# Kernel optimization log

Hardware: AMD Instinct MI355X
Metric: run time of the kernel (lower is better)

The kernel has to match this reference:

```python
import jax, jax.numpy as jnp
import numpy as np

B, N, C, H = 8, 512, 64, 128
T, K = 10, 2                       # dilation threshold and skip divisor
TAUS = (0.25, 0.5, 0.75)
WTS = (0.25, 0.5, 0.25)
EPS_GIN = 0.0                      # (1 + eps) * x, eps buffer
AVG_DEG = 32.0


def setup_inputs() -> dict:
    key = jax.random.key(0)
    ks = jax.random.split(key, 6)
    x = jax.random.normal(ks[0], (B, N, C), jnp.float32)
    u = jax.random.uniform(ks[1], (B, N, N))
    a = u < (AVG_DEG / N)
    adj = jnp.maximum(a, jnp.swapaxes(a, 1, 2)).astype(jnp.float32)  # symmetric binary adjacency
    mask = jax.random.bernoulli(ks[2], 0.9, (B, N))
    W1 = jax.random.normal(ks[3], (C, H), jnp.float32) / np.float32(np.sqrt(C))
    b1 = jnp.zeros((H,), jnp.float32)
    W2 = jax.random.normal(ks[4], (H, C), jnp.float32) / np.float32(np.sqrt(H))
    b2 = jnp.zeros((C,), jnp.float32)
    return {"x": x, "adj": adj, "mask": mask, "W1": W1, "b1": b1, "W2": W2, "b2": b2}


def reference(x, adj, mask, W1, b1, W2, b2):
    Bc, Nc, Cc = x.shape
    eye = jnp.eye(Nc, dtype=bool)
    adj_ = jnp.where(eye, 1.0, adj)                 # add_loop=True: force self loops
    # ---- vectorized dilation (replaces the per-(b,n) python loop) ----
    neigh = (adj_ > 0) & (~eye)                     # neighbors excluding self [B,N,N]
    ni = neigh.astype(jnp.int32)
    rank = jnp.cumsum(ni, axis=-1) - ni             # exclusive rank of m among n's sorted neighbors
    nb = ni.sum(-1)                                 # [B,N] neighbor count (w/o self)
    skip = jnp.where(nb > T, (nb + K - 1) // K, 1)  # ceil(nb/k) if nb > T else 1 (linear mode, layer 1)
    skip = jnp.maximum(skip, 1)
    sk = skip[:, :, None]
    # remove relative indices skip-1, 2*skip-1, ... when skip > 1, only for masked-in nodes
    rem = neigh & (sk > 1) & ((rank % sk) == (sk - 1)) & mask[:, :, None]
    rem = rem | jnp.swapaxes(rem, 1, 2)             # symmetric removal
    adj_d = jnp.where(rem, 0.0, adj_)
    # ---- masked quantile aggregation over neighbors (== nanquantile) ----
    nd = adj_d > 0                                  # includes self loop -> at least 1 valid
    vals = jnp.where(nd[..., None], x[:, None, :, :], jnp.inf)  # [B,N,M,C]; invalid -> +inf
    s = jnp.sort(vals, axis=2)                      # valid values first, ascending
    nv = nd.sum(2)                                  # [B,N] valid count per node
    agg = jnp.zeros_like(x)
    for tau, w in zip(TAUS, WTS):                   # small fixed loop over quantiles
        pos = jnp.asarray(tau, x.dtype) * jnp.maximum(nv - 1, 0).astype(x.dtype)
        lo = jnp.floor(pos).astype(jnp.int32)
        hi = jnp.ceil(pos).astype(jnp.int32)
        frac = (pos - lo.astype(x.dtype))[..., None]
        idx_lo = jnp.broadcast_to(lo[:, :, None, None], (Bc, Nc, 1, Cc))
        idx_hi = jnp.broadcast_to(hi[:, :, None, None], (Bc, Nc, 1, Cc))
        v_lo = jnp.take_along_axis(s, idx_lo, axis=2)[:, :, 0, :]
        v_hi = jnp.take_along_axis(s, idx_hi, axis=2)[:, :, 0, :]
        agg = agg + jnp.asarray(w, x.dtype) * (v_lo + frac * (v_hi - v_lo))
    agg = jnp.where(nv[..., None] > 0, agg, 0.0)    # nan_to_num for empty rows
    out = (1.0 + EPS_GIN) * x + agg
    h = jax.nn.relu(out @ W1 + b1)                  # GIN MLP: Linear-ReLU-Linear
    y = h @ W2 + b2
    return y * mask[..., None].astype(y.dtype)
```

## Files before the change

### kernel.cpp

```cpp
#include <hip/hip_runtime.h>
#include <cstdint>

#define B_ 8
#define N_ 512
#define C_ 64
#define H_ 128
#define T_ 10
#define K_ 2
#define WPR 16
#define NVMAX 96
#define TT 8

__device__ inline uint32_t fkey(float v) {
    uint32_t bits = __float_as_uint(v);
    return (bits & 0x80000000u) ? ~bits : (bits | 0x80000000u);
}
__device__ inline float fdec(uint32_t key) {
    uint32_t ok = (key & 0xFFFFFF00u) | 0x80u;
    uint32_t bits = (ok & 0x80000000u) ? (ok ^ 0x80000000u) : ~ok;
    return __uint_as_float(bits);
}

__global__ __launch_bounds__(256) void pass1_rem(const float* __restrict__ adj,
                                                 const int* __restrict__ mask,
                                                 uint32_t* __restrict__ rembits) {
    int wid = threadIdx.x >> 6, lane = threadIdx.x & 63;
    int row = blockIdx.x * 4 + wid;
    int i = row & (N_ - 1);
    const float4* arow4 = (const float4*)(adj + (size_t)row * N_);
    float4 a0 = arow4[lane * 2];
    float4 a1 = arow4[lane * 2 + 1];
    float av[8] = {a0.x, a0.y, a0.z, a0.w, a1.x, a1.y, a1.z, a1.w};

    int flags = 0, cnt = 0;
    int jbase = lane * 8;
#pragma unroll
    for (int k = 0; k < 8; ++k) {
        int j = jbase + k;
        bool ng = (j != i) && (av[k] > 0.0f);
        flags |= ((int)ng) << k;
        cnt += (int)ng;
    }
    int inc = cnt;
#pragma unroll
    for (int d = 1; d < 64; d <<= 1) {
        int o = __shfl_up(inc, d, 64);
        if (lane >= d) inc += o;
    }
    int excl = inc - cnt;
    int nb = __shfl(inc, 63, 64);
    int skip = (nb > T_) ? ((nb + K_ - 1) / K_) : 1;
    if (skip < 1) skip = 1;
    int maski = mask[row];

    unsigned byteval = 0;
    if (skip > 1 && maski != 0) {
        int r = excl;
#pragma unroll
        for (int k = 0; k < 8; ++k) {
            if ((flags >> k) & 1) {
                if (r % skip == skip - 1) byteval |= 1u << k;
                ++r;
            }
        }
    }
    unsigned b0 = __shfl((int)byteval, (lane & 15) * 4 + 0, 64);
    unsigned b1 = __shfl((int)byteval, (lane & 15) * 4 + 1, 64);
    unsigned b2 = __shfl((int)byteval, (lane & 15) * 4 + 2, 64);
    unsigned b3 = __shfl((int)byteval, (lane & 15) * 4 + 3, 64);
    if (lane < WPR) {
        uint32_t w = b0 | (b1 << 8) | (b2 << 16) | (b3 << 24);
        rembits[(size_t)row * WPR + lane] = w;
    }
}

__global__ __launch_bounds__(256) void pass2_quant_mlp(
        const float* __restrict__ x, const float* __restrict__ adj,
        const int* __restrict__ mask, const uint32_t* __restrict__ rembits,
        const float* __restrict__ W1, const float* __restrict__ b1,
        const float* __restrict__ W2, const float* __restrict__ b2,
        float* __restrict__ out) {
    int row = blockIdx.x;
    int b = row >> 9, i = row & (N_ - 1);
    int tid = threadIdx.x;
    int lane = tid & 63;
    int q = tid >> 6;

    __shared__ unsigned short kept[NVMAX];
    __shared__ int s_cnt;
    __shared__ uint32_t keys[NVMAX * C_];
    __shared__ float selv[6][C_];
    __shared__ int s_rr[6];
    __shared__ float s_frac[3];
    __shared__ float out_node[C_];
    __shared__ float hbuf[H_];

    if (tid == 0) s_cnt = 0;
    __syncthreads();

    const float* arow = adj + (size_t)row * N_;
    const uint32_t* rrow = rembits + (size_t)row * WPR;
    const uint32_t* rbase = rembits + (size_t)(b * N_) * WPR;

    for (int jb = 0; jb < N_; jb += 256) {
        int j = jb + tid;
        bool keep;
        if (j == i) {
            keep = true;
        } else {
            keep = (arow[j] > 0.0f);
            if (keep) {
                unsigned rij = (rrow[j >> 5] >> (j & 31)) & 1u;
                unsigned rji = (rbase[(size_t)j * WPR + (i >> 5)] >> (i & 31)) & 1u;
                keep = ((rij | rji) == 0u);
            }
        }
        unsigned long long bal = __ballot(keep);
        int base = 0;
        if (lane == 0 && bal) base = atomicAdd(&s_cnt, __popcll(bal));
        base = __shfl(base, 0, 64);
        if (keep) {
            int pos = __popcll(bal & ((1ull << lane) - 1ull));
            int p = base + pos;
            if (p < NVMAX) kept[p] = (unsigned short)j;
        }
    }
    __syncthreads();
    int nv = s_cnt;
    if (nv > NVMAX) nv = NVMAX;

    const float* xb = x + (size_t)b * N_ * C_;

    for (int t = q; t < nv; t += 4) {
        float v = xb[(size_t)kept[t] * C_ + lane];
        keys[t * C_ + lane] = (fkey(v) & 0xFFFFFF00u) | (uint32_t)t;
    }

    if (tid == 0) {
        const float taus[3] = {0.25f, 0.5f, 0.75f};
        float nm1 = (float)((nv - 1 > 0) ? nv - 1 : 0);
        for (int qq = 0; qq < 3; ++qq) {
            float pos = taus[qq] * nm1;
            int lo = (int)floorf(pos);
            int hi = (int)ceilf(pos);
            s_rr[2 * qq] = lo; s_rr[2 * qq + 1] = hi;
            s_frac[qq] = pos - (float)lo;
        }
    }
    __syncthreads();

    int rr0 = s_rr[0], rr1 = s_rr[1], rr2 = s_rr[2],
        rr3 = s_rr[3], rr4 = s_rr[4], rr5 = s_rr[5];

    const uint32_t* kcol = keys + lane;

    for (int base = 0; base < nv; base += 32) {
        int tbase = base + q * TT;
        if (tbase >= nv) continue;
        uint32_t k[TT];
        int rs_a[TT], rs_b[TT];
#pragma unroll
        for (int m = 0; m < TT; ++m) {
            int t = tbase + m;
            k[m] = (t < nv) ? kcol[t * C_] : 0xFFFFFFFFu;
            rs_a[m] = 0; rs_b[m] = 0;
        }
        int u = 0;
#pragma unroll 2
        for (; u + 1 < nv; u += 2) {
            uint32_t w0 = kcol[u * C_];
            uint32_t w1 = kcol[(u + 1) * C_];
#pragma unroll
            for (int m = 0; m < TT; ++m) {
                rs_a[m] += (int)(w0 < k[m]);
                rs_b[m] += (int)(w1 < k[m]);
            }
        }
        if (u < nv) {
            uint32_t w0 = kcol[u * C_];
#pragma unroll
            for (int m = 0; m < TT; ++m) rs_a[m] += (int)(w0 < k[m]);
        }
#pragma unroll
        for (int m = 0; m < TT; ++m) {
            int rs = rs_a[m] + rs_b[m];
            bool h0 = rs == rr0, h1 = rs == rr1, h2 = rs == rr2;
            bool h3 = rs == rr3, h4 = rs == rr4, h5 = rs == rr5;
            if (h0 | h1 | h2 | h3 | h4 | h5) {
                float fv = fdec(k[m]);
                if (h0) selv[0][lane] = fv;
                if (h1) selv[1][lane] = fv;
                if (h2) selv[2][lane] = fv;
                if (h3) selv[3][lane] = fv;
                if (h4) selv[4][lane] = fv;
                if (h5) selv[5][lane] = fv;
            }
        }
    }
    __syncthreads();

    if (tid < C_) {
        float f0 = s_frac[0], f1 = s_frac[1], f2 = s_frac[2];
        float agg = 0.25f * (selv[0][tid] + f0 * (selv[1][tid] - selv[0][tid]));
        agg      += 0.5f  * (selv[2][tid] + f1 * (selv[3][tid] - selv[2][tid]));
        agg      += 0.25f * (selv[4][tid] + f2 * (selv[5][tid] - selv[4][tid]));
        out_node[tid] = xb[(size_t)i * C_ + tid] + agg;
    }
    __syncthreads();

    float maskf = (mask[row] != 0) ? 1.0f : 0.0f;
    if (tid < H_) {
        float acc = b1[tid];
        for (int c = 0; c < C_; ++c) acc += out_node[c] * W1[c * H_ + tid];
        hbuf[tid] = acc > 0.0f ? acc : 0.0f;
    }
    __syncthreads();
    if (tid < C_) {
        float acc = b2[tid];
        for (int k = 0; k < H_; ++k) acc += hbuf[k] * W2[k * C_ + tid];
        out[(size_t)row * C_ + tid] = acc * maskf;
    }
}

extern "C" void kernel_launch(void* const* d_in, const int* in_sizes, int n_in,
                              void* d_out, int out_size, void* d_ws, size_t ws_size,
                              hipStream_t stream) {
    const float* x   = (const float*)d_in[0];
    const float* adj = (const float*)d_in[1];
    const int*  mask = (const int*)d_in[2];
    const float* W1  = (const float*)d_in[3];
    const float* b1  = (const float*)d_in[4];
    const float* W2  = (const float*)d_in[5];
    const float* b2  = (const float*)d_in[6];
    float* out = (float*)d_out;

    uint32_t* rembits = (uint32_t*)d_ws;

    hipLaunchKernelGGL(pass1_rem, dim3(B_ * N_ / 4), dim3(256), 0, stream,
                       adj, mask, rembits);
    hipLaunchKernelGGL(pass2_quant_mlp, dim3(B_ * N_), dim3(256), 0, stream,
                       x, adj, mask, rembits, W1, b1, W2, b2, out);
}
```

Baseline: 165.6 us.

## Split MLP across all threads, widen rank tile, drop modulo in removal scan

Both MLP layers now run on all 256 threads, each dot product split across 2 or 4 threads and combined with shuffle reductions. Before, only 128 or 64 threads worked while the rest sat idle. The rank-counting tile grows from 8 to 16 keys per thread, so each pass covers 64 candidates, fewer passes over shared keys are needed, and register use rises. The per-element modulo in pass1 becomes a running counter, and the self feature is loaded early to hide its latency.

```diff
diff --git a/kernel.cpp b/kernel.cpp
--- a/kernel.cpp
+++ b/kernel.cpp
@@ -9,7 +9,7 @@
 #define K_ 2
 #define WPR 16
 #define NVMAX 96
-#define TT 8
+#define TT 16
 
 __device__ inline uint32_t fkey(float v) {
     uint32_t bits = __float_as_uint(v);
@@ -55,12 +55,12 @@
 
     unsigned byteval = 0;
     if (skip > 1 && maski != 0) {
-        int r = excl;
+        int r = excl % skip;
 #pragma unroll
         for (int k = 0; k < 8; ++k) {
             if ((flags >> k) & 1) {
-                if (r % skip == skip - 1) byteval |= 1u << k;
-                ++r;
+                if (r == skip - 1) { byteval |= 1u << k; r = 0; }
+                else ++r;
             }
         }
     }
@@ -147,6 +147,9 @@
             s_frac[qq] = pos - (float)lo;
         }
     }
+
+    float xself = 0.0f;
+    if (q == 0) xself = xb[(size_t)i * C_ + lane];
     __syncthreads();
 
     int rr0 = s_rr[0], rr1 = s_rr[1], rr2 = s_rr[2],
@@ -154,7 +157,7 @@
 
     const uint32_t* kcol = keys + lane;
 
-    for (int base = 0; base < nv; base += 32) {
+    for (int base = 0; base < nv; base += 64) {
         int tbase = base + q * TT;
         if (tbase >= nv) continue;
         uint32_t k[TT];
@@ -204,21 +207,36 @@
         float agg = 0.25f * (selv[0][tid] + f0 * (selv[1][tid] - selv[0][tid]));
         agg      += 0.5f  * (selv[2][tid] + f1 * (selv[3][tid] - selv[2][tid]));
         agg      += 0.25f * (selv[4][tid] + f2 * (selv[5][tid] - selv[4][tid]));
-        out_node[tid] = xb[(size_t)i * C_ + tid] + agg;
+        out_node[tid] = xself + agg;
     }
     __syncthreads();
 
     float maskf = (mask[row] != 0) ? 1.0f : 0.0f;
-    if (tid < H_) {
-        float acc = b1[tid];
-        for (int c = 0; c < C_; ++c) acc += out_node[c] * W1[c * H_ + tid];
-        hbuf[tid] = acc > 0.0f ? acc : 0.0f;
-    }
-    __syncthreads();
-    if (tid < C_) {
-        float acc = b2[tid];
-        for (int k = 0; k < H_; ++k) acc += hbuf[k] * W2[k * C_ + tid];
-        out[(size_t)row * C_ + tid] = acc * maskf;
+    {
+        int h = tid >> 1, half = tid & 1;
+        int c0 = half * 32;
+        float acc = 0.0f;
+#pragma unroll 4
+        for (int c = 0; c < 32; ++c)
+            acc += out_node[c0 + c] * W1[(size_t)(c0 + c) * H_ + h];
+        acc += __shfl_xor(acc, 1, 64);
+        if (half == 0) {
+            float v = acc + b1[h];
+            hbuf[h] = v > 0.0f ? v : 0.0f;
+        }
+    }
+    __syncthreads();
+    {
+        int c = tid >> 2, quad = tid & 3;
+        int k0 = quad * 32;
+        float acc = 0.0f;
+#pragma unroll 4
+        for (int k = 0; k < 32; ++k)
+            acc += hbuf[k0 + k] * W2[(size_t)(k0 + k) * C_ + c];
+        acc += __shfl_xor(acc, 1, 64);
+        acc += __shfl_xor(acc, 2, 64);
+        if (quad == 0)
+            out[(size_t)row * C_ + c] = (acc + b2[c]) * maskf;
     }
 }
 
```

New measurement: 182.1 us. +10.0%, slower.
